# Kernel optimization log

Hardware: AMD Instinct MI355X
Metric: run time of the kernel (lower is better)

The kernel has to match this reference:

```python
import jax, jax.numpy as jnp
import numpy as np

N_NODES = 32768   # graph.num_nodes (coarse + fine levels)
N_ACTIVE = 28672  # rows of x (finest level)
N_EDGES = 229376  # avg degree ~7 (h3 k_ring + parent links)
C = 64            # node_channels
E_CH = 2          # edge_channels
HID = 128         # hidden_channels
L = 8             # num_layers


def _ln(x, g, b):
    # LayerNorm over last dim, eps=1e-5 (torch default)
    m = jnp.mean(x, axis=-1, keepdims=True)
    v = jnp.mean((x - m) ** 2, axis=-1, keepdims=True)
    return (x - m) * jax.lax.rsqrt(v + 1e-5) * g + b


def _ffn(x, w1, b1, w2, b2, g, bln, res_w=None, res_b=None):
    # FFN: norm(residual(x) + Linear-ReLU-Linear(x)); residual is Identity if in==out
    res = x @ res_w + res_b if res_w is not None else x
    h = jax.nn.relu(x @ w1 + b1) @ w2 + b2
    return _ln(res + h, g, bln)


def setup_inputs() -> dict:
    key = jax.random.key(0)
    ks = iter(jax.random.split(key, 64))

    def W(*s):
        return (0.02 * jax.random.normal(next(ks), s)).astype(jnp.float32)

    inp = {}
    inp['x'] = jax.random.normal(next(ks), (N_ACTIVE, C), jnp.float32)
    inp['edge_index'] = jax.random.randint(next(ks), (2, N_EDGES), 0, N_NODES)
    inp['edge_attr'] = jax.random.uniform(next(ks), (N_EDGES, E_CH), jnp.float32)
    # EdgeModel FFN: in = 2*C + E_CH -> out = E_CH (residual Linear since in != out)
    ein = 2 * C + E_CH
    inp['e_res_w'] = W(L, ein, E_CH); inp['e_res_b'] = jnp.zeros((L, E_CH), jnp.float32)
    inp['e_w1'] = W(L, ein, HID);     inp['e_b1'] = jnp.zeros((L, HID), jnp.float32)
    inp['e_w2'] = W(L, HID, E_CH);    inp['e_b2'] = jnp.zeros((L, E_CH), jnp.float32)
    inp['e_ln_g'] = jnp.ones((L, E_CH), jnp.float32); inp['e_ln_b'] = jnp.zeros((L, E_CH), jnp.float32)
    # NodeModel mlp_1: in = out = C + E_CH (residual Identity)
    m1 = C + E_CH
    inp['n1_w1'] = W(L, m1, HID);  inp['n1_b1'] = jnp.zeros((L, HID), jnp.float32)
    inp['n1_w2'] = W(L, HID, m1);  inp['n1_b2'] = jnp.zeros((L, m1), jnp.float32)
    inp['n1_ln_g'] = jnp.ones((L, m1), jnp.float32); inp['n1_ln_b'] = jnp.zeros((L, m1), jnp.float32)
    # NodeModel mlp_2: in = 2*C + E_CH -> out = C (residual Linear)
    inp['n2_res_w'] = W(L, ein, C); inp['n2_res_b'] = jnp.zeros((L, C), jnp.float32)
    inp['n2_w1'] = W(L, ein, HID);  inp['n2_b1'] = jnp.zeros((L, HID), jnp.float32)
    inp['n2_w2'] = W(L, HID, C);    inp['n2_b2'] = jnp.zeros((L, C), jnp.float32)
    inp['n2_ln_g'] = jnp.ones((L, C), jnp.float32); inp['n2_ln_b'] = jnp.zeros((L, C), jnp.float32)
    return inp


def reference(x, edge_index, edge_attr,
              e_res_w, e_res_b, e_w1, e_b1, e_w2, e_b2, e_ln_g, e_ln_b,
              n1_w1, n1_b1, n1_w2, n1_b2, n1_ln_g, n1_ln_b,
              n2_res_w, n2_res_b, n2_w1, n2_b1, n2_w2, n2_b2, n2_ln_g, n2_ln_b):
    pad = N_NODES - x.shape[0]
    nodes = jnp.concatenate([jnp.zeros((pad, x.shape[1]), x.dtype), x], axis=0)
    edges = edge_attr
    row, col = edge_index[0], edge_index[1]
    # per-node in-degree for scatter-mean (clamped to 1 so isolated nodes get 0)
    cnt = jnp.maximum(
        jax.ops.segment_sum(jnp.ones((N_EDGES,), x.dtype), col, num_segments=N_NODES), 1.0
    )[:, None]
    for l in range(L):
        src = nodes[row]   # [E, C]
        dst = nodes[col]   # [E, C]
        # EdgeModel: edge_mlp(cat(src, dest, edge_attr)) + edge_attr
        edges = _ffn(jnp.concatenate([src, dst, edges], axis=1),
                     e_w1[l], e_b1[l], e_w2[l], e_b2[l], e_ln_g[l], e_ln_b[l],
                     e_res_w[l], e_res_b[l]) + edges
        # NodeModel: mlp1 on cat(x[row], edge_attr), scatter-mean onto col
        m = _ffn(jnp.concatenate([src, edges], axis=1),
                 n1_w1[l], n1_b1[l], n1_w2[l], n1_b2[l], n1_ln_g[l], n1_ln_b[l])
        agg = jax.ops.segment_sum(m, col, num_segments=N_NODES) / cnt
        nodes = _ffn(jnp.concatenate([nodes, agg], axis=1),
                     n2_w1[l], n2_b1[l], n2_w2[l], n2_b2[l], n2_ln_g[l], n2_ln_b[l],
                     n2_res_w[l], n2_res_b[l]) + nodes
    return nodes[pad:]
```

## Files before the change

### kernel.cpp

```cpp
#include <hip/hip_runtime.h>

#define NN    32768
#define NACT  28672
#define NPAD  4096
#define NEDGE 229376
#define NLAY  8

#define WOFF_T0 0
#define WOFF_T1 18432
#define WOFF_T2 26624
#define WOFF_T3 36864
#define WOFF_T4 61440
#define WLO     69632
#define WLAYER  139264

typedef __attribute__((ext_vector_type(8))) short s16x8;
typedef __attribute__((ext_vector_type(8))) _Float16 f16x8;
typedef __attribute__((ext_vector_type(4))) float f32x4;
typedef unsigned short ushort_t;

#define MFMAH(a,b,c) __builtin_amdgcn_mfma_f32_16x16x32_f16((a),(b),(c),0,0,0)
#define INV2048 4.8828125e-4f

__device__ __forceinline__ unsigned short f2h(float f){
  union { _Float16 h; unsigned short u; } v; v.h = (_Float16)f; return v.u;
}
__device__ __forceinline__ float h2f(unsigned short u){
  union { unsigned short u; _Float16 h; } v; v.u = u; return (float)v.h;
}
__device__ __forceinline__ void split16(float a, unsigned short& h, unsigned short& r){
  float hf = 0.f; unsigned short hu = 0;
  if (__builtin_fabsf(a) >= 6.1035156e-5f){ hu = f2h(a); hf = h2f(hu); }
  h = hu;
  r = f2h((a - hf) * 2048.0f);
}
__device__ __forceinline__ void split8v(const float* v, s16x8& h, s16x8& r){
  #pragma unroll
  for (int i=0;i<8;++i){
    unsigned short hh, rr; split16(v[i], hh, rr);
    h[i] = (short)hh; r[i] = (short)rr;
  }
}

__global__ void k_pack(const float* __restrict__ ew1, const float* __restrict__ eresw,
                       const float* __restrict__ n1w1, const float* __restrict__ n1w2,
                       const float* __restrict__ n2w1, const float* __restrict__ n2resw,
                       const float* __restrict__ n2w2,
                       unsigned short* __restrict__ wfrag){
  const int l = blockIdx.y, T = blockIdx.z;
  int KT, NT, off;
  if (T==0){ KT=4; NT=9;  off=WOFF_T0; }
  else if (T==1){ KT=2; NT=8;  off=WOFF_T1; }
  else if (T==2){ KT=4; NT=5;  off=WOFF_T2; }
  else if (T==3){ KT=4; NT=12; off=WOFF_T3; }
  else          { KT=4; NT=4;  off=WOFF_T4; }
  const int f = blockIdx.x*256 + threadIdx.x;
  if (f >= KT*NT*64) return;
  const int lane = f & 63;
  const int fn = f >> 6;
  const int nt = fn % NT, ks = fn / NT;
  const int n  = nt*16 + (lane & 15);
  const int kb = ks*32 + (lane >> 4)*8;
  s16x8 vh, vl;
  #pragma unroll
  for (int i=0;i<8;++i){
    const int k = kb + i;
    float w = 0.f;
    if (T==0){
      if (n < 128)      w = ew1[((size_t)l*130 + k)*128 + n];
      else if (n < 130) w = eresw[((size_t)l*130 + k)*2 + (n-128)];
    } else if (T==1){
      w = n1w1[((size_t)l*66 + k)*128 + n];
    } else if (T==2){
      if (n < 66) w = n1w2[((size_t)l*128 + k)*66 + n];
    } else if (T==3){
      if (n < 128) w = n2w1[((size_t)l*130 + k)*128 + n];
      else         w = n2resw[((size_t)l*130 + k)*64 + (n-128)];
    } else {
      w = n2w2[((size_t)l*128 + k)*64 + n];
    }
    unsigned short hh, rr; split16(w, hh, rr);
    vh[i] = (short)hh; vl[i] = (short)rr;
  }
  *(s16x8*)(wfrag + (size_t)l*WLAYER + off + (size_t)f*8) = vh;
  *(s16x8*)(wfrag + (size_t)l*WLAYER + off + WLO + (size_t)f*8) = vl;
}

__global__ void k_init(const float* __restrict__ x, const float* __restrict__ ea,
                       float* __restrict__ nodes, float* __restrict__ edges,
                       int* __restrict__ cnt,
                       ushort_t* __restrict__ nh, ushort_t* __restrict__ nr){
  const int i = blockIdx.x*256 + threadIdx.x;
  const float v = (i >= NPAD*64) ? x[i - NPAD*64] : 0.f;
  nodes[i] = v;
  if (nh){
    unsigned short us, ur; split16(v, us, ur);
    nh[i] = us; nr[i] = ur;
  }
  if (i < NEDGE*2) edges[i] = ea[i];
  if (i < NN) cnt[i] = 0;
}

__global__ void k_count(const int* __restrict__ ei, int* __restrict__ cnt){
  const int e = blockIdx.x*256 + threadIdx.x;
  if (e < NEDGE) atomicAdd(&cnt[ei[NEDGE + e]], 1);
}

__global__ void k_inv(const int* __restrict__ cnt, float* __restrict__ invc,
                      int* __restrict__ fill){
  const int n = blockIdx.x*256 + threadIdx.x;
  if (n < NN){ invc[n] = 1.0f / (float)max(cnt[n], 1); fill[n] = 0; }
}

__global__ void k_scan(const int* __restrict__ cnt, int* __restrict__ row_start){
  __shared__ int part[256];
  const int t = threadIdx.x;
  int s = 0;
  for (int i=0;i<128;++i) s += cnt[t*128+i];
  part[t] = s;
  __syncthreads();
  if (t == 0){
    int run = 0;
    for (int i=0;i<256;++i){ const int v = part[i]; part[i] = run; run += v; }
  }
  __syncthreads();
  int base = part[t];
  for (int i=0;i<128;++i){ row_start[t*128+i] = base; base += cnt[t*128+i]; }
  if (t == 255) row_start[NN] = base;
}

__global__ void k_place(const int* __restrict__ ei, const int* __restrict__ row_start,
                        int* __restrict__ fill, int* __restrict__ ssrc,
                        int* __restrict__ sdst, int* __restrict__ seid){
  const int e = blockIdx.x*256 + threadIdx.x;
  if (e >= NEDGE) return;
  const int d = ei[NEDGE + e];
  const int pos = row_start[d] + atomicAdd(&fill[d], 1);
  ssrc[pos] = ei[e];
  sdst[pos] = d;
  seid[pos] = e;
}

__global__ void k_sortb(const int* __restrict__ row_start,
                        int* __restrict__ seid, int* __restrict__ ssrc){
  const int n = blockIdx.x*256 + threadIdx.x;
  if (n >= NN) return;
  const int rs = row_start[n], re = row_start[n+1];
  for (int i = rs+1; i < re; ++i){
    const int e = seid[i], s = ssrc[i];
    int j = i-1;
    while (j >= rs && seid[j] > e){ seid[j+1]=seid[j]; ssrc[j+1]=ssrc[j]; --j; }
    seid[j+1] = e; ssrc[j+1] = s;
  }
}

__global__ void k_perm(const float* __restrict__ ea, const int* __restrict__ seid,
                       float* __restrict__ edges){
  const int e = blockIdx.x*256 + threadIdx.x;
  if (e < NEDGE){
    const int o = seid[e];
    ((float2*)edges)[e] = ((const float2*)ea)[o];
  }
}

__global__ void k_zero_agg(float* __restrict__ agg64, float* __restrict__ agg2){
  const int i = blockIdx.x*256 + threadIdx.x;
  agg64[i] = 0.f;
  if (i < NN*2) agg2[i] = 0.f;
}

__global__ __launch_bounds__(256)
void k_agg(const float* __restrict__ medge64, const float* __restrict__ medge2,
           const int* __restrict__ row_start, const int* __restrict__ cnt,
           ushort_t* __restrict__ agg_h, ushort_t* __restrict__ agg_r,
           float* __restrict__ agg2){
  const int n = blockIdx.x*4 + (threadIdx.x >> 6);
  const int lane = threadIdx.x & 63;
  const int rs = row_start[n], re = row_start[n+1];
  const float cf = (float)max(cnt[n], 1);
  float a = 0.f, b = 0.f;
  for (int r = rs; r < re; ++r){
    a = __fadd_rn(a, medge64[(size_t)r*64 + lane]);
    if (lane < 2) b = __fadd_rn(b, medge2[(size_t)r*2 + lane]);
  }
  const float t = a / cf;
  unsigned short th, tr; split16(t, th, tr);
  agg_h[(size_t)n*64 + lane] = th;
  agg_r[(size_t)n*64 + lane] = tr;
  if (lane < 2) agg2[(size_t)n*2 + lane] = b / cf;
}

__global__ __launch_bounds__(256,3)
void k_edge(const int* __restrict__ sidx, const int* __restrict__ didx,
            float* __restrict__ edges,
            const float* __restrict__ nodes,
            const ushort_t* __restrict__ nh, const ushort_t* __restrict__ nr,
            const unsigned short* __restrict__ wf,
            float* __restrict__ agg64, float* __restrict__ agg2,
            float* __restrict__ medge64, float* __restrict__ medge2,
            const float* __restrict__ eb1, const float* __restrict__ ew2,
            const float* __restrict__ eb2, const float* __restrict__ eresb,
            const float* __restrict__ elng, const float* __restrict__ elnb,
            const float* __restrict__ ew1_tail,
            const float* __restrict__ eresw_tail,
            const float* __restrict__ n1w1_tail,
            const float* __restrict__ n1b1, const float* __restrict__ n1b2,
            const float* __restrict__ n1lng, const float* __restrict__ n1lnb)
{
  __shared__ __align__(16) unsigned char sAh[64*128];
  __shared__ __align__(16) unsigned char sAl[64*128];
  __shared__ __align__(16) unsigned char sBH[64*256];
  __shared__ __align__(16) unsigned char sH2l[64*256];
  __shared__ float sEold[64][2];
  __shared__ int   sCol[64];

  const int tid = threadIdx.x;
  const int ebase = blockIdx.x * 64;

  {
    const int r = (tid & 127) >> 1;
    const int half = tid & 1;
    const int es = ebase + r;
    const int swz = (r & 7) << 4;
    if (tid < 128){
      const int sn = sidx[es];
      if (nh){
        const ushort_t* hp = nh + (size_t)sn*64;
        const ushort_t* rp = nr + (size_t)sn*64;
        #pragma unroll
        for (int cc = 0; cc < 4; ++cc){
          const int c = half*4 + cc;
          const int o = r*128 + ((c*16) ^ swz);
          *(s16x8*)&sAh[o] = *(const s16x8*)(hp + c*8);
          *(s16x8*)&sAl[o] = *(const s16x8*)(rp + c*8);
        }
      } else {
        const float4* sp = (const float4*)(nodes + (size_t)sn*64);
        #pragma unroll
        for (int cc = 0; cc < 4; ++cc){
          const int c = half*4 + cc;
          const float4 f0 = sp[2*c], f1 = sp[2*c+1];
          float v[8] = {f0.x,f0.y,f0.z,f0.w,f1.x,f1.y,f1.z,f1.w};
          s16x8 hh, rr; split8v(v, hh, rr);
          const int o = r*128 + ((c*16) ^ swz);
          *(s16x8*)&sAh[o] = hh;
          *(s16x8*)&sAl[o] = rr;
        }
      }
    } else {
      const int dn = didx[es];
      if (nh){
        const ushort_t* hp = nh + (size_t)dn*64;
        const ushort_t* rp = nr + (size_t)dn*64;
        #pragma unroll
        for (int cc = 0; cc < 4; ++cc){
          const int c = half*4 + cc;
          const int o = r*128 + ((c*16) ^ swz);
          *(s16x8*)&sBH[o] = *(const s16x8*)(hp + c*8);
          *(s16x8*)&sBH[8192 + o] = *(const s16x8*)(rp + c*8);
        }
      } else {
        const float4* dp = (const float4*)(nodes + (size_t)dn*64);
        #pragma unroll
        for (int cc = 0; cc < 4; ++cc){
          const int c = half*4 + cc;
          const float4 f0 = dp[2*c], f1 = dp[2*c+1];
          float v[8] = {f0.x,f0.y,f0.z,f0.w,f1.x,f1.y,f1.z,f1.w};
          s16x8 hh, rr; split8v(v, hh, rr);
          const int o = r*128 + ((c*16) ^ swz);
          *(s16x8*)&sBH[o] = hh;
          *(s16x8*)&sBH[8192 + o] = rr;
        }
      }
      if (half == 0){
        const float2 ev = *(const float2*)(edges + (size_t)es*2);
        sEold[r][0] = ev.x; sEold[r][1] = ev.y;
        sCol[r] = dn;
      }
    }
  }
  __syncthreads();

  const int lane  = tid & 63;
  const int wv    = tid >> 6;
  const int colj  = lane & 15;
  const int g     = lane >> 4;
  const int rowA0 = wv*16 + colj;
  const int mrow0 = wv*16 + g*4;

  float e0r[4], e1r[4];
  #pragma unroll
  for (int r=0; r<4; ++r){
    const int m = mrow0 + r;
    e0r[r] = sEold[m][0]; e1r[r] = sEold[m][1];
  }

  f32x4 acc1[9];
  #pragma unroll
  for (int i=0;i<9;++i) acc1[i] = f32x4{0,0,0,0};
  {
    #pragma unroll
    for (int half = 0; half < 2; ++half){
      const int nt0 = half*5;
      const int NTH = half ? 4 : 5;
      f32x4 accR[5];
      #pragma unroll
      for (int i=0;i<5;++i) accR[i] = f32x4{0,0,0,0};
      #pragma unroll
      for (int ks = 0; ks < 4; ++ks){
        const int ch = (ks&1)*4 + g;
        const unsigned char* pH = (ks<2) ? sAh : sBH;
        const unsigned char* pL = (ks<2) ? sAl : (sBH + 8192);
        const int o0 = rowA0*128 + ((ch*16) ^ ((rowA0&7)<<4));
        const f16x8 ah = *(const f16x8*)&pH[o0];
        const f16x8 ar = *(const f16x8*)&pL[o0];
        const f16x8* bh = (const f16x8*)(wf + WOFF_T0) + (ks*9 + nt0)*64 + lane;
        const f16x8* bl = (const f16x8*)(wf + WOFF_T0 + WLO) + (ks*9 + nt0)*64 + lane;
        #pragma unroll
        for (int t = 0; t < 5; ++t){
          if (t >= NTH) break;
          const f16x8 b1 = bh[t*64];
          const f16x8 b2 = bl[t*64];
          acc1[nt0+t] = MFMAH(ah, b1, acc1[nt0+t]);
          accR[t]     = MFMAH(ar, b1, accR[t]);
          accR[t]     = MFMAH(ah, b2, accR[t]);
        }
      }
      #pragma unroll
      for (int t=0; t<5; ++t){
        if (t >= NTH) break;
        #pragma unroll
        for (int r=0; r<4; ++r)
          acc1[nt0+t][r] += accR[t][r] * INV2048;
      }
    }
    #pragma unroll
    for (int nt=0; nt<9; ++nt){
      const int j = nt*16 + colj;
      float w0, w1;
      if (nt < 8){ w0 = ew1_tail[j]; w1 = ew1_tail[128 + j]; }
      else { w0 = (colj<2) ? eresw_tail[colj] : 0.f; w1 = (colj<2) ? eresw_tail[2+colj] : 0.f; }
      #pragma unroll
      for (int r=0; r<4; ++r)
        acc1[nt][r] += e0r[r]*w0 + e1r[r]*w1;
    }
  }

  float enew[4][2];
  {
    float2 w2v[8]; float b1v[8];
    #pragma unroll
    for (int nt=0; nt<8; ++nt){
      const int j = nt*16 + colj;
      w2v[nt] = *(const float2*)(ew2 + (size_t)j*2);
      b1v[nt] = eb1[j];
    }
    const float rb0 = eresb[0], rb1 = eresb[1];
    const float g0 = elng[0], g1 = elng[1], lb0 = elnb[0], lb1 = elnb[1];
    const float bb0 = eb2[0], bb1 = eb2[1];
    #pragma unroll
    for (int r=0; r<4; ++r){
      float v0 = 0.f, v1 = 0.f;
      #pragma unroll
      for (int nt=0; nt<8; ++nt){
        const float h = fmaxf(acc1[nt][r] + b1v[nt], 0.f);
        v0 = fmaf(h, w2v[nt].x, v0);
        v1 = fmaf(h, w2v[nt].y, v1);
      }
      const float resv = acc1[8][r];
      if (colj == 0) v0 += resv + rb0;
      if (colj == 1) v1 += resv + rb1;
      #pragma unroll
      for (int mm=1; mm<16; mm<<=1){
        v0 += __shfl_xor(v0, mm, 64);
        v1 += __shfl_xor(v1, mm, 64);
      }
      v0 += bb0; v1 += bb1;
      const float m2 = __fmul_rn(__fadd_rn(v0, v1), 0.5f);
      const float d0 = __fsub_rn(v0, m2);
      const float d1 = __fsub_rn(v1, m2);
      const float var = __fmul_rn(__fadd_rn(__fmul_rn(d0,d0), __fmul_rn(d1,d1)), 0.5f);
      const float rstd = 1.0f / sqrtf(var + 1e-5f);
      const int m = mrow0 + r;
      const float e0 = __fadd_rn(__fadd_rn(__fmul_rn(__fmul_rn(d0, rstd), g0), lb0), e0r[r]);
      const float e1 = __fadd_rn(__fadd_rn(__fmul_rn(__fmul_rn(d1, rstd), g1), lb1), e1r[r]);
      enew[r][0] = e0; enew[r][1] = e1;
      if (colj == 0)
        *(float2*)(edges + (size_t)(ebase + m)*2) = make_float2(e0, e1);
    }
  }

  f32x4 acc2[8];
  #pragma unroll
  for (int i=0;i<8;++i) acc2[i] = f32x4{0,0,0,0};
  {
    #pragma unroll
    for (int half = 0; half < 2; ++half){
      const int nt0 = half*4;
      f32x4 accR[4];
      #pragma unroll
      for (int i=0;i<4;++i) accR[i] = f32x4{0,0,0,0};
      #pragma unroll
      for (int ks=0; ks<2; ++ks){
        const int ch = ks*4 + g;
        const int o0 = rowA0*128 + ((ch*16) ^ ((rowA0&7)<<4));
        const f16x8 ah = *(const f16x8*)&sAh[o0];
        const f16x8 ar = *(const f16x8*)&sAl[o0];
        const f16x8* bh = (const f16x8*)(wf + WOFF_T1) + (ks*8 + nt0)*64 + lane;
        const f16x8* bl = (const f16x8*)(wf + WOFF_T1 + WLO) + (ks*8 + nt0)*64 + lane;
        #pragma unroll
        for (int t = 0; t < 4; ++t){
          const f16x8 b1 = bh[t*64];
          const f16x8 b2 = bl[t*64];
          acc2[nt0+t] = MFMAH(ah, b1, acc2[nt0+t]);
          accR[t]     = MFMAH(ar, b1, accR[t]);
          accR[t]     = MFMAH(ah, b2, accR[t]);
        }
      }
      #pragma unroll
      for (int t=0; t<4; ++t)
        #pragma unroll
        for (int r=0; r<4; ++r)
          acc2[nt0+t][r] += accR[t][r] * INV2048;
    }
  }
  {
    #pragma unroll
    for (int nt=0; nt<8; ++nt){
      const int j = nt*16 + colj;
      const float w64 = n1w1_tail[j];
      const float w65 = n1w1_tail[128 + j];
      const float bb = n1b1[j];
      #pragma unroll
      for (int r=0; r<4; ++r){
        float h = acc2[nt][r] + enew[r][0]*w64 + enew[r][1]*w65 + bb;
        acc2[nt][r] = fmaxf(h, 0.f);
      }
    }
  }

  __syncthreads();

  {
    #pragma unroll
    for (int nt=0; nt<8; ++nt){
      const int j = nt*16 + colj;
      const int co = (j>>3)<<4, wi = (j&7)*2;
      #pragma unroll
      for (int r=0; r<4; ++r){
        const int m = mrow0 + r;
        unsigned short us, ur; split16(acc2[nt][r], us, ur);
        const int o = m*256 + ((co ^ ((m&7)<<4)) + wi);
        *(unsigned short*)&sBH[o]  = us;
        *(unsigned short*)&sH2l[o] = ur;
      }
    }
  }
  __syncthreads();

  f32x4 acc3[5], acc3R[5];
  #pragma unroll
  for (int i=0;i<5;++i){ acc3[i] = f32x4{0,0,0,0}; acc3R[i] = f32x4{0,0,0,0}; }
  #pragma unroll
  for (int ks=0; ks<4; ++ks){
    const int ch = ks*4 + g;
    const f16x8 a0 = *(const f16x8*)&sBH[rowA0*256 + ((ch*16) ^ ((rowA0&7)<<4))];
    const f16x8* bh = (const f16x8*)(wf + WOFF_T2) + (ks*5)*64 + lane;
    const f16x8* bl = (const f16x8*)(wf + WOFF_T2 + WLO) + (ks*5)*64 + lane;
    #pragma unroll
    for (int nt = 0; nt < 5; ++nt){
      const f16x8 b1 = bh[nt*64];
      const f16x8 b2 = bl[nt*64];
      acc3[nt]  = MFMAH(a0, b1, acc3[nt]);
      acc3R[nt] = MFMAH(a0, b2, acc3R[nt]);
    }
  }
  #pragma unroll
  for (int ks=0; ks<4; ++ks){
    const int ch = ks*4 + g;
    const f16x8 a0 = *(const f16x8*)&sH2l[rowA0*256 + ((ch*16) ^ ((rowA0&7)<<4))];
    const f16x8* bh = (const f16x8*)(wf + WOFF_T2) + (ks*5)*64 + lane;
    #pragma unroll
    for (int nt = 0; nt < 5; ++nt){
      const f16x8 b1 = bh[nt*64];
      acc3R[nt] = MFMAH(a0, b1, acc3R[nt]);
    }
  }
  #pragma unroll
  for (int nt=0; nt<5; ++nt)
    #pragma unroll
    for (int r=0; r<4; ++r)
      acc3[nt][r] += acc3R[nt][r] * INV2048;

  {
    float b2v[5], lgv[5], lbv[5];
    #pragma unroll
    for (int nt=0; nt<5; ++nt){
      const int j = nt*16 + colj;
      const bool ok = j < 66;
      b2v[nt] = ok ? n1b2[j]  : 0.f;
      lgv[nt] = ok ? n1lng[j] : 0.f;
      lbv[nt] = ok ? n1lnb[j] : 0.f;
    }
    #pragma unroll
    for (int r=0; r<4; ++r){
      const int m = mrow0 + r;
      float v[5]; float sum = 0.f;
      #pragma unroll
      for (int nt=0; nt<5; ++nt){
        const int j = nt*16 + colj;
        float xv = 0.f;
        if (j < 64){
          const int o = m*128 + (((((j>>3)<<4)) ^ ((m&7)<<4)) + (j&7)*2);
          const float resd = h2f(*(const unsigned short*)&sAh[o])
                           + h2f(*(const unsigned short*)&sAl[o]) * INV2048;
          xv = __fadd_rn(resd, __fadd_rn(acc3[nt][r], b2v[nt]));
        } else if (j < 66){
          xv = __fadd_rn(enew[r][j-64], __fadd_rn(acc3[nt][r], b2v[nt]));
        }
        v[nt] = xv;
        sum += xv;
      }
      #pragma unroll
      for (int mm=1; mm<16; mm<<=1) sum += __shfl_xor(sum, mm, 64);
      const float mean = sum / 66.0f;
      float d[5]; float sq = 0.f;
      #pragma unroll
      for (int nt=0; nt<5; ++nt){
        const int j = nt*16 + colj;
        d[nt] = (j < 66) ? __fsub_rn(v[nt], mean) : 0.f;
        sq = __fadd_rn(sq, __fmul_rn(d[nt], d[nt]));
      }
      #pragma unroll
      for (int mm=1; mm<16; mm<<=1) sq += __shfl_xor(sq, mm, 64);
      const float var  = sq / 66.0f;
      const float rstd = 1.0f / sqrtf(var + 1e-5f);
      if (medge64){
        float* m64 = medge64 + (size_t)(ebase + m)*64;
        #pragma unroll
        for (int nt=0; nt<4; ++nt)
          m64[nt*16 + colj] = __fadd_rn(__fmul_rn(__fmul_rn(d[nt], rstd), lgv[nt]), lbv[nt]);
        if (colj < 2)
          medge2[(size_t)(ebase + m)*2 + colj] =
            __fadd_rn(__fmul_rn(__fmul_rn(d[4], rstd), lgv[4]), lbv[4]);
      } else {
        float* a64 = agg64 + (size_t)sCol[m]*64;
        #pragma unroll
        for (int nt=0; nt<4; ++nt)
          atomicAdd(a64 + nt*16 + colj, __fadd_rn(__fmul_rn(__fmul_rn(d[nt], rstd), lgv[nt]), lbv[nt]));
        if (colj < 2)
          atomicAdd(agg2 + (size_t)sCol[m]*2 + colj,
                    __fadd_rn(__fmul_rn(__fmul_rn(d[4], rstd), lgv[4]), lbv[4]));
      }
    }
  }
}

__global__ __launch_bounds__(256,3)
void k_node(float* __restrict__ nodes,
            ushort_t* __restrict__ nh, ushort_t* __restrict__ nr,
            const float* __restrict__ agg64,
            const ushort_t* __restrict__ agg_h, const ushort_t* __restrict__ agg_r,
            const float* __restrict__ agg2,
            const float* __restrict__ invc,
            const unsigned short* __restrict__ wf,
            const float* __restrict__ b1, const float* __restrict__ resb,
            const float* __restrict__ b2, const float* __restrict__ lng,
            const float* __restrict__ lnb,
            const float* __restrict__ n2w1_tail,
            const float* __restrict__ n2resw_tail)
{
  __shared__ __align__(16) unsigned char sAh[64*128];
  __shared__ __align__(16) unsigned char sAl[64*128];
  __shared__ __align__(16) unsigned char sBH[64*256];
  __shared__ __align__(16) unsigned char sH3l[64*256];
  __shared__ float sAgg2[64][2];

  const int tid = threadIdx.x;
  const int nbase = blockIdx.x * 64;

  {
    const int r = (tid & 127) >> 1;
    const int half = tid & 1;
    const int node = nbase + r;
    const int swz = (r & 7) << 4;
    if (tid < 128){
      if (nh){
        const ushort_t* hp = nh + (size_t)node*64;
        const ushort_t* rp = nr + (size_t)node*64;
        #pragma unroll
        for (int cc = 0; cc < 4; ++cc){
          const int c = half*4 + cc;
          const int o = r*128 + ((c*16) ^ swz);
          *(s16x8*)&sAh[o] = *(const s16x8*)(hp + c*8);
          *(s16x8*)&sAl[o] = *(const s16x8*)(rp + c*8);
        }
      } else {
        const float4* sp = (const float4*)(nodes + (size_t)node*64);
        #pragma unroll
        for (int cc = 0; cc < 4; ++cc){
          const int c = half*4 + cc;
          const float4 f0 = sp[2*c], f1 = sp[2*c+1];
          float v[8] = {f0.x,f0.y,f0.z,f0.w,f1.x,f1.y,f1.z,f1.w};
          s16x8 hh, rr; split8v(v, hh, rr);
          const int o = r*128 + ((c*16) ^ swz);
          *(s16x8*)&sAh[o] = hh;
          *(s16x8*)&sAl[o] = rr;
        }
      }
    } else {
      if (agg_h){
        const ushort_t* hp = agg_h + (size_t)node*64;
        const ushort_t* rp = agg_r + (size_t)node*64;
        #pragma unroll
        for (int cc = 0; cc < 4; ++cc){
          const int c = half*4 + cc;
          const int o = r*128 + ((c*16) ^ swz);
          *(s16x8*)&sBH[o] = *(const s16x8*)(hp + c*8);
          *(s16x8*)&sBH[8192 + o] = *(const s16x8*)(rp + c*8);
        }
        if (half == 0){
          sAgg2[r][0] = agg2[(size_t)node*2];
          sAgg2[r][1] = agg2[(size_t)node*2+1];
        }
      } else {
        const float iv = invc[node];
        const float* a64 = agg64 + (size_t)node*64;
        #pragma unroll
        for (int cc = 0; cc < 4; ++cc){
          const int c = half*4 + cc;
          float v[8];
          #pragma unroll
          for (int i=0;i<8;++i) v[i] = a64[c*8+i]*iv;
          s16x8 hh, rr; split8v(v, hh, rr);
          const int o = r*128 + ((c*16) ^ swz);
          *(s16x8*)&sBH[o] = hh;
          *(s16x8*)&sBH[8192 + o] = rr;
        }
        if (half == 0){
          sAgg2[r][0] = agg2[(size_t)node*2]*iv;
          sAgg2[r][1] = agg2[(size_t)node*2+1]*iv;
        }
      }
    }
  }
  __syncthreads();

  const int lane  = tid & 63;
  const int wv    = tid >> 6;
  const int colj  = lane & 15;
  const int g     = lane >> 4;
  const int rowA0 = wv*16 + colj;
  const int mrow0 = wv*16 + g*4;

  float a0r[4], a1r[4];
  #pragma unroll
  for (int r=0; r<4; ++r){
    const int m = mrow0 + r;
    a0r[r] = sAgg2[m][0]; a1r[r] = sAgg2[m][1];
  }

  f32x4 acc1[12];
  #pragma unroll
  for (int i=0;i<12;++i) acc1[i] = f32x4{0,0,0,0};
  #pragma unroll
  for (int half = 0; half < 2; ++half){
    f32x4 aR[6];
    #pragma unroll
    for (int i=0;i<6;++i) aR[i] = f32x4{0,0,0,0};
    #pragma unroll
    for (int ks = 0; ks < 4; ++ks){
      const int ch = (ks&1)*4 + g;
      const unsigned char* pH = (ks<2) ? sAh : sBH;
      const unsigned char* pL = (ks<2) ? sAl : (sBH + 8192);
      const int o0 = rowA0*128 + ((ch*16) ^ ((rowA0&7)<<4));
      const f16x8 ah = *(const f16x8*)&pH[o0];
      const f16x8 ar = *(const f16x8*)&pL[o0];
      const f16x8* bh = (const f16x8*)(wf + WOFF_T3) + (ks*12 + half*6)*64 + lane;
      const f16x8* bl = (const f16x8*)(wf + WOFF_T3 + WLO) + (ks*12 + half*6)*64 + lane;
      #pragma unroll
      for (int t = 0; t < 6; ++t){
        const int nt = half*6 + t;
        const f16x8 b1 = bh[t*64];
        const f16x8 b2 = bl[t*64];
        acc1[nt] = MFMAH(ah, b1, acc1[nt]);
        aR[t]    = MFMAH(ar, b1, aR[t]);
        aR[t]    = MFMAH(ah, b2, aR[t]);
      }
    }
    #pragma unroll
    for (int t=0;t<6;++t)
      #pragma unroll
      for (int r=0; r<4; ++r)
        acc1[half*6+t][r] += aR[t][r] * INV2048;
  }
  {
    #pragma unroll
    for (int nt=0; nt<12; ++nt){
      const int j = nt*16 + colj;
      float w0, w1;
      if (j < 128){ w0 = n2w1_tail[j]; w1 = n2w1_tail[128 + j]; }
      else { w0 = n2resw_tail[j-128]; w1 = n2resw_tail[64 + (j-128)]; }
      #pragma unroll
      for (int r=0; r<4; ++r)
        acc1[nt][r] += a0r[r]*w0 + a1r[r]*w1;
    }
  }
  {
    #pragma unroll
    for (int nt=0; nt<8; ++nt){
      const float bb = b1[nt*16 + colj];
      #pragma unroll
      for (int r=0; r<4; ++r)
        acc1[nt][r] = fmaxf(acc1[nt][r] + bb, 0.f);
    }
  }

  __syncthreads();

  {
    #pragma unroll
    for (int nt=0; nt<8; ++nt){
      const int j = nt*16 + colj;
      const int co = (j>>3)<<4, wi = (j&7)*2;
      #pragma unroll
      for (int r=0; r<4; ++r){
        const int m = mrow0 + r;
        unsigned short us, ur; split16(acc1[nt][r], us, ur);
        const int o = m*256 + ((co ^ ((m&7)<<4)) + wi);
        *(unsigned short*)&sBH[o]  = us;
        *(unsigned short*)&sH3l[o] = ur;
      }
    }
  }
  __syncthreads();

  f32x4 acc2[4], acc2R[4];
  #pragma unroll
  for (int i=0;i<4;++i){ acc2[i] = f32x4{0,0,0,0}; acc2R[i] = f32x4{0,0,0,0}; }
  #pragma unroll
  for (int ks=0; ks<4; ++ks){
    const int ch = ks*4 + g;
    const f16x8 a0 = *(const f16x8*)&sBH[rowA0*256 + ((ch*16) ^ ((rowA0&7)<<4))];
    const f16x8* bh = (const f16x8*)(wf + WOFF_T4) + (ks*4)*64 + lane;
    const f16x8* bl = (const f16x8*)(wf + WOFF_T4 + WLO) + (ks*4)*64 + lane;
    #pragma unroll
    for (int nt = 0; nt < 4; ++nt){
      const f16x8 b1 = bh[nt*64];
      const f16x8 b2 = bl[nt*64];
      acc2[nt]  = MFMAH(a0, b1, acc2[nt]);
      acc2R[nt] = MFMAH(a0, b2, acc2R[nt]);
    }
  }
  #pragma unroll
  for (int ks=0; ks<4; ++ks){
    const int ch = ks*4 + g;
    const f16x8 a0 = *(const f16x8*)&sH3l[rowA0*256 + ((ch*16) ^ ((rowA0&7)<<4))];
    const f16x8* bh = (const f16x8*)(wf + WOFF_T4) + (ks*4)*64 + lane;
    #pragma unroll
    for (int nt = 0; nt < 4; ++nt){
      const f16x8 b1 = bh[nt*64];
      acc2R[nt] = MFMAH(a0, b1, acc2R[nt]);
    }
  }
  #pragma unroll
  for (int nt=0; nt<4; ++nt)
    #pragma unroll
    for (int r=0; r<4; ++r)
      acc2[nt][r] += acc2R[nt][r] * INV2048;

  {
    float b2v[4], rbv[4], lgv[4], lbv[4];
    #pragma unroll
    for (int nt=0; nt<4; ++nt){
      const int j = nt*16 + colj;
      b2v[nt] = b2[j]; rbv[nt] = resb[j]; lgv[nt] = lng[j]; lbv[nt] = lnb[j];
    }
    #pragma unroll
    for (int r=0; r<4; ++r){
      const int m = mrow0 + r;
      const int node = nbase + m;
      float v[4]; float sum = 0.f;
      #pragma unroll
      for (int nt=0; nt<4; ++nt){
        const float resi = __fadd_rn(acc1[8+nt][r], rbv[nt]);
        const float hh   = __fadd_rn(acc2[nt][r], b2v[nt]);
        const float xv = __fadd_rn(resi, hh);
        v[nt] = xv; sum += xv;
      }
      #pragma unroll
      for (int mm=1; mm<16; mm<<=1) sum += __shfl_xor(sum, mm, 64);
      const float mean = sum / 64.0f;
      float d[4]; float sq = 0.f;
      #pragma unroll
      for (int nt=0; nt<4; ++nt){
        d[nt] = __fsub_rn(v[nt], mean);
        sq = __fadd_rn(sq, __fmul_rn(d[nt], d[nt]));
      }
      #pragma unroll
      for (int mm=1; mm<16; mm<<=1) sq += __shfl_xor(sq, mm, 64);
      const float var  = sq / 64.0f;
      const float rstd = 1.0f / sqrtf(var + 1e-5f);
      #pragma unroll
      for (int nt=0; nt<4; ++nt){
        const int j = nt*16 + colj;
        const size_t idx = (size_t)node*64 + j;
        const float lnout = __fadd_rn(__fmul_rn(__fmul_rn(d[nt], rstd), lgv[nt]), lbv[nt]);
        const float out = __fadd_rn(lnout, nodes[idx]);
        nodes[idx] = out;
        if (nh){
          unsigned short us, ur; split16(out, us, ur);
          nh[idx] = us; nr[idx] = ur;
        }
      }
    }
  }
}

__global__ void k_copy(const float* __restrict__ nodes, float* __restrict__ out){
  const int i = blockIdx.x*256 + threadIdx.x;
  if (i < NACT*16)
    ((float4*)out)[i] = ((const float4*)nodes)[NPAD*16 + i];
}

extern "C" void kernel_launch(void* const* d_in, const int* in_sizes, int n_in,
                              void* d_out, int out_size, void* d_ws, size_t ws_size,
                              hipStream_t stream){
  const float* x       = (const float*)d_in[0];
  const int*   ei      = (const int*)  d_in[1];
  const float* eattr   = (const float*)d_in[2];
  const float* e_res_w = (const float*)d_in[3];
  const float* e_res_b = (const float*)d_in[4];
  const float* e_w1    = (const float*)d_in[5];
  const float* e_b1    = (const float*)d_in[6];
  const float* e_w2    = (const float*)d_in[7];
  const float* e_b2    = (const float*)d_in[8];
  const float* e_ln_g  = (const float*)d_in[9];
  const float* e_ln_b  = (const float*)d_in[10];
  const float* n1_w1   = (const float*)d_in[11];
  const float* n1_b1   = (const float*)d_in[12];
  const float* n1_w2   = (const float*)d_in[13];
  const float* n1_b2   = (const float*)d_in[14];
  const float* n1_ln_g = (const float*)d_in[15];
  const float* n1_ln_b = (const float*)d_in[16];
  const float* n2_res_w= (const float*)d_in[17];
  const float* n2_res_b= (const float*)d_in[18];
  const float* n2_w1   = (const float*)d_in[19];
  const float* n2_b1   = (const float*)d_in[20];
  const float* n2_w2   = (const float*)d_in[21];
  const float* n2_b2   = (const float*)d_in[22];
  const float* n2_ln_g = (const float*)d_in[23];
  const float* n2_ln_b = (const float*)d_in[24];

  if (ws_size < 21364736u) return;

  char* ws = (char*)d_ws;
  float*          nodes = (float*)(ws + 0);
  float*          edges = (float*)(ws + 8388608);
  float*          agg64 = (float*)(ws + 10223616);
  ushort_t*       agg_h = (ushort_t*)(ws + 10223616);
  ushort_t*       agg_r = (ushort_t*)(ws + 14417920);
  float*          agg2  = (float*)(ws + 18612224);
  int*            cnt   = (int*)(ws + 18874368);
  float*          invc  = (float*)(ws + 19005440);
  unsigned short* wfrag = (unsigned short*)(ws + 19136512);
  int*   row_start = (int*)(ws + 21364736);
  int*   fill      = (int*)(ws + 21496064);
  int*   ssrc      = (int*)(ws + 21627136);
  int*   sdst      = (int*)(ws + 22544640);
  int*   seid      = (int*)(ws + 23462144);
  float* medge64   = (float*)(ws + 24379648);
  float* medge2    = (float*)(ws + 83099904);
  ushort_t* nodes_h = (ushort_t*)(ws + 84934912);
  ushort_t* nodes_r = (ushort_t*)(ws + 89129216);

  const bool fast  = ws_size >= 84934912u;
  const bool fast2 = ws_size >= 93323520u;

  ushort_t* nh = fast2 ? nodes_h : nullptr;
  ushort_t* nr = fast2 ? nodes_r : nullptr;

  k_pack<<<dim3(12,8,5),256,0,stream>>>(e_w1, e_res_w, n1_w1, n1_w2, n2_w1, n2_res_w, n2_w2, wfrag);
  k_init<<<8192,256,0,stream>>>(x, eattr, nodes, edges, cnt, nh, nr);
  k_count<<<896,256,0,stream>>>(ei, cnt);
  k_inv<<<128,256,0,stream>>>(cnt, invc, fast ? fill : cnt );

  const int* sidx = ei;
  const int* didx = ei + NEDGE;
  if (fast){
    k_scan<<<1,256,0,stream>>>(cnt, row_start);
    k_place<<<896,256,0,stream>>>(ei, row_start, fill, ssrc, sdst, seid);
    k_sortb<<<128,256,0,stream>>>(row_start, seid, ssrc);
    k_perm<<<896,256,0,stream>>>(eattr, seid, edges);
    sidx = ssrc; didx = sdst;
  }

  for (int l = 0; l < NLAY; ++l){
    if (!fast) k_zero_agg<<<8192,256,0,stream>>>(agg64, agg2);
    k_edge<<<3584,256,0,stream>>>(sidx, didx, edges, nodes, nh, nr,
        wfrag + (size_t)l*WLAYER, agg64, agg2,
        fast ? medge64 : nullptr, fast ? medge2 : nullptr,
        e_b1 + l*128, e_w2 + l*256, e_b2 + l*2, e_res_b + l*2, e_ln_g + l*2, e_ln_b + l*2,
        e_w1 + ((size_t)l*130 + 128)*128,
        e_res_w + ((size_t)l*130 + 128)*2,
        n1_w1 + ((size_t)l*66 + 64)*128,
        n1_b1 + l*128, n1_b2 + l*66, n1_ln_g + l*66, n1_ln_b + l*66);
    if (fast) k_agg<<<8192,256,0,stream>>>(medge64, medge2, row_start, cnt, agg_h, agg_r, agg2);
    k_node<<<512,256,0,stream>>>(nodes, nh, nr,
        fast ? nullptr : agg64,
        fast ? agg_h : nullptr, fast ? agg_r : nullptr, agg2,
        fast ? nullptr : invc,
        wfrag + (size_t)l*WLAYER,
        n2_b1 + l*128, n2_res_b + l*64, n2_b2 + l*64, n2_ln_g + l*64, n2_ln_b + l*64,
        n2_w1 + ((size_t)l*130 + 128)*128,
        n2_res_w + ((size_t)l*130 + 128)*64);
  }
  k_copy<<<1792,256,0,stream>>>(nodes, (float*)d_out);
}
```

Baseline: 1.367 ms.

## Fuse CSR aggregation into node kernel and halve LDS to raise occupancy

Measured after the change: 1.843 ms. 1.35x slower.

```diff
diff --git a/kernel.cpp b/kernel.cpp
--- a/kernel.cpp
+++ b/kernel.cpp
@@ -169,28 +169,7 @@
   if (i < NN*2) agg2[i] = 0.f;
 }
 
-__global__ __launch_bounds__(256)
-void k_agg(const float* __restrict__ medge64, const float* __restrict__ medge2,
-           const int* __restrict__ row_start, const int* __restrict__ cnt,
-           ushort_t* __restrict__ agg_h, ushort_t* __restrict__ agg_r,
-           float* __restrict__ agg2){
-  const int n = blockIdx.x*4 + (threadIdx.x >> 6);
-  const int lane = threadIdx.x & 63;
-  const int rs = row_start[n], re = row_start[n+1];
-  const float cf = (float)max(cnt[n], 1);
-  float a = 0.f, b = 0.f;
-  for (int r = rs; r < re; ++r){
-    a = __fadd_rn(a, medge64[(size_t)r*64 + lane]);
-    if (lane < 2) b = __fadd_rn(b, medge2[(size_t)r*2 + lane]);
-  }
-  const float t = a / cf;
-  unsigned short th, tr; split16(t, th, tr);
-  agg_h[(size_t)n*64 + lane] = th;
-  agg_r[(size_t)n*64 + lane] = tr;
-  if (lane < 2) agg2[(size_t)n*2 + lane] = b / cf;
-}
-
-__global__ __launch_bounds__(256,3)
+__global__ __launch_bounds__(256,4)
 void k_edge(const int* __restrict__ sidx, const int* __restrict__ didx,
             float* __restrict__ edges,
             const float* __restrict__ nodes,
@@ -209,8 +188,8 @@
 {
   __shared__ __align__(16) unsigned char sAh[64*128];
   __shared__ __align__(16) unsigned char sAl[64*128];
-  __shared__ __align__(16) unsigned char sBH[64*256];
-  __shared__ __align__(16) unsigned char sH2l[64*256];
+  __shared__ __align__(16) unsigned char sBh[64*128];
+  __shared__ __align__(16) unsigned char sBl[64*128];
   __shared__ float sEold[64][2];
   __shared__ int   sCol[64];
 
@@ -256,8 +235,8 @@
         for (int cc = 0; cc < 4; ++cc){
           const int c = half*4 + cc;
           const int o = r*128 + ((c*16) ^ swz);
-          *(s16x8*)&sBH[o] = *(const s16x8*)(hp + c*8);
-          *(s16x8*)&sBH[8192 + o] = *(const s16x8*)(rp + c*8);
+          *(s16x8*)&sBh[o] = *(const s16x8*)(hp + c*8);
+          *(s16x8*)&sBl[o] = *(const s16x8*)(rp + c*8);
         }
       } else {
         const float4* dp = (const float4*)(nodes + (size_t)dn*64);
@@ -268,8 +247,8 @@
           float v[8] = {f0.x,f0.y,f0.z,f0.w,f1.x,f1.y,f1.z,f1.w};
           s16x8 hh, rr; split8v(v, hh, rr);
           const int o = r*128 + ((c*16) ^ swz);
-          *(s16x8*)&sBH[o] = hh;
-          *(s16x8*)&sBH[8192 + o] = rr;
+          *(s16x8*)&sBh[o] = hh;
+          *(s16x8*)&sBl[o] = rr;
         }
       }
       if (half == 0){
@@ -309,8 +288,8 @@
       #pragma unroll
       for (int ks = 0; ks < 4; ++ks){
         const int ch = (ks&1)*4 + g;
-        const unsigned char* pH = (ks<2) ? sAh : sBH;
-        const unsigned char* pL = (ks<2) ? sAl : (sBH + 8192);
+        const unsigned char* pH = (ks<2) ? sAh : sBh;
+        const unsigned char* pL = (ks<2) ? sAl : sBl;
         const int o0 = rowA0*128 + ((ch*16) ^ ((rowA0&7)<<4));
         const f16x8 ah = *(const f16x8*)&pH[o0];
         const f16x8 ar = *(const f16x8*)&pL[o0];
@@ -439,51 +418,44 @@
     }
   }
 
-  __syncthreads();
-
-  {
-    #pragma unroll
-    for (int nt=0; nt<8; ++nt){
-      const int j = nt*16 + colj;
-      const int co = (j>>3)<<4, wi = (j&7)*2;
+  f32x4 acc3[5], acc3R[5];
+  #pragma unroll
+  for (int i=0;i<5;++i){ acc3[i] = f32x4{0,0,0,0}; acc3R[i] = f32x4{0,0,0,0}; }
+  #pragma unroll
+  for (int c = 0; c < 2; ++c){
+    __syncthreads();
+    #pragma unroll
+    for (int ntl=0; ntl<4; ++ntl){
+      const int nt = c*4 + ntl;
+      const int jc = ntl*16 + colj;
+      const int co = (jc>>3)<<4, wi = (jc&7)*2;
       #pragma unroll
       for (int r=0; r<4; ++r){
         const int m = mrow0 + r;
         unsigned short us, ur; split16(acc2[nt][r], us, ur);
-        const int o = m*256 + ((co ^ ((m&7)<<4)) + wi);
-        *(unsigned short*)&sBH[o]  = us;
-        *(unsigned short*)&sH2l[o] = ur;
-      }
-    }
-  }
-  __syncthreads();
-
-  f32x4 acc3[5], acc3R[5];
-  #pragma unroll
-  for (int i=0;i<5;++i){ acc3[i] = f32x4{0,0,0,0}; acc3R[i] = f32x4{0,0,0,0}; }
-  #pragma unroll
-  for (int ks=0; ks<4; ++ks){
-    const int ch = ks*4 + g;
-    const f16x8 a0 = *(const f16x8*)&sBH[rowA0*256 + ((ch*16) ^ ((rowA0&7)<<4))];
-    const f16x8* bh = (const f16x8*)(wf + WOFF_T2) + (ks*5)*64 + lane;
-    const f16x8* bl = (const f16x8*)(wf + WOFF_T2 + WLO) + (ks*5)*64 + lane;
-    #pragma unroll
-    for (int nt = 0; nt < 5; ++nt){
-      const f16x8 b1 = bh[nt*64];
-      const f16x8 b2 = bl[nt*64];
-      acc3[nt]  = MFMAH(a0, b1, acc3[nt]);
-      acc3R[nt] = MFMAH(a0, b2, acc3R[nt]);
-    }
-  }
-  #pragma unroll
-  for (int ks=0; ks<4; ++ks){
-    const int ch = ks*4 + g;
-    const f16x8 a0 = *(const f16x8*)&sH2l[rowA0*256 + ((ch*16) ^ ((rowA0&7)<<4))];
-    const f16x8* bh = (const f16x8*)(wf + WOFF_T2) + (ks*5)*64 + lane;
-    #pragma unroll
-    for (int nt = 0; nt < 5; ++nt){
-      const f16x8 b1 = bh[nt*64];
-      acc3R[nt] = MFMAH(a0, b1, acc3R[nt]);
+        const int o = m*128 + ((co ^ ((m&7)<<4)) + wi);
+        *(unsigned short*)&sBh[o] = us;
+        *(unsigned short*)&sBl[o] = ur;
+      }
+    }
+    __syncthreads();
+    #pragma unroll
+    for (int ksl=0; ksl<2; ++ksl){
+      const int ks = c*2 + ksl;
+      const int ch = ksl*4 + g;
+      const int o0 = rowA0*128 + ((ch*16) ^ ((rowA0&7)<<4));
+      const f16x8 ah = *(const f16x8*)&sBh[o0];
+      const f16x8 al = *(const f16x8*)&sBl[o0];
+      const f16x8* bh = (const f16x8*)(wf + WOFF_T2) + (ks*5)*64 + lane;
+      const f16x8* bl = (const f16x8*)(wf + WOFF_T2 + WLO) + (ks*5)*64 + lane;
+      #pragma unroll
+      for (int nt = 0; nt < 5; ++nt){
+        const f16x8 b1 = bh[nt*64];
+        const f16x8 b2 = bl[nt*64];
+        acc3[nt]  = MFMAH(ah, b1, acc3[nt]);
+        acc3R[nt] = MFMAH(ah, b2, acc3R[nt]);
+        acc3R[nt] = MFMAH(al, b1, acc3R[nt]);
+      }
     }
   }
   #pragma unroll
@@ -556,12 +528,12 @@
   }
 }
 
-__global__ __launch_bounds__(256,3)
+__global__ __launch_bounds__(256,4)
 void k_node(float* __restrict__ nodes,
             ushort_t* __restrict__ nh, ushort_t* __restrict__ nr,
-            const float* __restrict__ agg64,
-            const ushort_t* __restrict__ agg_h, const ushort_t* __restrict__ agg_r,
-            const float* __restrict__ agg2,
+            const float* __restrict__ medge64, const float* __restrict__ medge2,
+            const int* __restrict__ row_start, const int* __restrict__ cntp,
+            const float* __restrict__ agg64, const float* __restrict__ agg2,
             const float* __restrict__ invc,
             const unsigned short* __restrict__ wf,
             const float* __restrict__ b1, const float* __restrict__ resb,
@@ -572,8 +544,8 @@
 {
   __shared__ __align__(16) unsigned char sAh[64*128];
   __shared__ __align__(16) unsigned char sAl[64*128];
-  __shared__ __align__(16) unsigned char sBH[64*256];
-  __shared__ __align__(16) unsigned char sH3l[64*256];
+  __shared__ __align__(16) unsigned char sBh[64*128];
+  __shared__ __align__(16) unsigned char sBl[64*128];
   __shared__ float sAgg2[64][2];
 
   const int tid = threadIdx.x;
@@ -609,19 +581,36 @@
         }
       }
     } else {
-      if (agg_h){
-        const ushort_t* hp = agg_h + (size_t)node*64;
-        const ushort_t* rp = agg_r + (size_t)node*64;
+      if (medge64){
+        const int rs = row_start[node], re = row_start[node+1];
+        const float cf = (float)max(cntp[node], 1);
         #pragma unroll
         for (int cc = 0; cc < 4; ++cc){
           const int c = half*4 + cc;
+          float a[8];
+          #pragma unroll
+          for (int i=0;i<8;++i) a[i] = 0.f;
+          for (int rr = rs; rr < re; ++rr){
+            const float* mr = medge64 + (size_t)rr*64 + c*8;
+            #pragma unroll
+            for (int i=0;i<8;++i) a[i] = __fadd_rn(a[i], mr[i]);
+          }
+          float v[8];
+          #pragma unroll
+          for (int i=0;i<8;++i) v[i] = a[i] / cf;
+          s16x8 hh, rr2; split8v(v, hh, rr2);
           const int o = r*128 + ((c*16) ^ swz);
-          *(s16x8*)&sBH[o] = *(const s16x8*)(hp + c*8);
-          *(s16x8*)&sBH[8192 + o] = *(const s16x8*)(rp + c*8);
+          *(s16x8*)&sBh[o] = hh;
+          *(s16x8*)&sBl[o] = rr2;
         }
         if (half == 0){
-          sAgg2[r][0] = agg2[(size_t)node*2];
-          sAgg2[r][1] = agg2[(size_t)node*2+1];
+          float b0 = 0.f, b1s = 0.f;
+          for (int rr = rs; rr < re; ++rr){
+            b0  = __fadd_rn(b0,  medge2[(size_t)rr*2]);
+            b1s = __fadd_rn(b1s, medge2[(size_t)rr*2+1]);
+          }
+          sAgg2[r][0] = b0 / cf;
+          sAgg2[r][1] = b1s / cf;
         }
       } else {
         const float iv = invc[node];
@@ -634,8 +623,8 @@
           for (int i=0;i<8;++i) v[i] = a64[c*8+i]*iv;
           s16x8 hh, rr; split8v(v, hh, rr);
           const int o = r*128 + ((c*16) ^ swz);
-          *(s16x8*)&sBH[o] = hh;
-          *(s16x8*)&sBH[8192 + o] = rr;
+          *(s16x8*)&sBh[o] = hh;
+          *(s16x8*)&sBl[o] = rr;
         }
         if (half == 0){
           sAgg2[r][0] = agg2[(size_t)node*2]*iv;
@@ -671,8 +660,8 @@
     #pragma unroll
     for (int ks = 0; ks < 4; ++ks){
       const int ch = (ks&1)*4 + g;
-      const unsigned char* pH = (ks<2) ? sAh : sBH;
-      const unsigned char* pL = (ks<2) ? sAl : (sBH + 8192);
+      const unsigned char* pH = (ks<2) ? sAh : sBh;
+      const unsigned char* pL = (ks<2) ? sAl : sBl;
       const int o0 = rowA0*128 + ((ch*16) ^ ((rowA0&7)<<4));
       const f16x8 ah = *(const f16x8*)&pH[o0];
       const f16x8 ar = *(const f16x8*)&pL[o0];
@@ -716,51 +705,44 @@
     }
   }
 
-  __syncthreads();
-
-  {
-    #pragma unroll
-    for (int nt=0; nt<8; ++nt){
-      const int j = nt*16 + colj;
-      const int co = (j>>3)<<4, wi = (j&7)*2;
+  f32x4 acc2[4], acc2R[4];
+  #pragma unroll
+  for (int i=0;i<4;++i){ acc2[i] = f32x4{0,0,0,0}; acc2R[i] = f32x4{0,0,0,0}; }
+  #pragma unroll
+  for (int c = 0; c < 2; ++c){
+    __syncthreads();
+    #pragma unroll
+    for (int ntl=0; ntl<4; ++ntl){
+      const int nt = c*4 + ntl;
+      const int jc = ntl*16 + colj;
+      const int co = (jc>>3)<<4, wi = (jc&7)*2;
       #pragma unroll
       for (int r=0; r<4; ++r){
         const int m = mrow0 + r;
         unsigned short us, ur; split16(acc1[nt][r], us, ur);
-        const int o = m*256 + ((co ^ ((m&7)<<4)) + wi);
-        *(unsigned short*)&sBH[o]  = us;
-        *(unsigned short*)&sH3l[o] = ur;
-      }
-    }
-  }
-  __syncthreads();
-
-  f32x4 acc2[4], acc2R[4];
-  #pragma unroll
-  for (int i=0;i<4;++i){ acc2[i] = f32x4{0,0,0,0}; acc2R[i] = f32x4{0,0,0,0}; }
-  #pragma unroll
-  for (int ks=0; ks<4; ++ks){
-    const int ch = ks*4 + g;
-    const f16x8 a0 = *(const f16x8*)&sBH[rowA0*256 + ((ch*16) ^ ((rowA0&7)<<4))];
-    const f16x8* bh = (const f16x8*)(wf + WOFF_T4) + (ks*4)*64 + lane;
-    const f16x8* bl = (const f16x8*)(wf + WOFF_T4 + WLO) + (ks*4)*64 + lane;
-    #pragma unroll
-    for (int nt = 0; nt < 4; ++nt){
-      const f16x8 b1 = bh[nt*64];
-      const f16x8 b2 = bl[nt*64];
-      acc2[nt]  = MFMAH(a0, b1, acc2[nt]);
-      acc2R[nt] = MFMAH(a0, b2, acc2R[nt]);
-    }
-  }
-  #pragma unroll
-  for (int ks=0; ks<4; ++ks){
-    const int ch = ks*4 + g;
-    const f16x8 a0 = *(const f16x8*)&sH3l[rowA0*256 + ((ch*16) ^ ((rowA0&7)<<4))];
-    const f16x8* bh = (const f16x8*)(wf + WOFF_T4) + (ks*4)*64 + lane;
-    #pragma unroll
-    for (int nt = 0; nt < 4; ++nt){
-      const f16x8 b1 = bh[nt*64];
-      acc2R[nt] = MFMAH(a0, b1, acc2R[nt]);
+        const int o = m*128 + ((co ^ ((m&7)<<4)) + wi);
+        *(unsigned short*)&sBh[o] = us;
+        *(unsigned short*)&sBl[o] = ur;
+      }
+    }
+    __syncthreads();
+    #pragma unroll
+    for (int ksl=0; ksl<2; ++ksl){
+      const int ks = c*2 + ksl;
+      const int ch = ksl*4 + g;
+      const int o0 = rowA0*128 + ((ch*16) ^ ((rowA0&7)<<4));
+      const f16x8 ah = *(const f16x8*)&sBh[o0];
+      const f16x8 al = *(const f16x8*)&sBl[o0];
+      const f16x8* bh = (const f16x8*)(wf + WOFF_T4) + (ks*4)*64 + lane;
+      const f16x8* bl = (const f16x8*)(wf + WOFF_T4 + WLO) + (ks*4)*64 + lane;
+      #pragma unroll
+      for (int nt = 0; nt < 4; ++nt){
+        const f16x8 b1 = bh[nt*64];
+        const f16x8 b2 = bl[nt*64];
+        acc2[nt]  = MFMAH(ah, b1, acc2[nt]);
+        acc2R[nt] = MFMAH(ah, b2, acc2R[nt]);
+        acc2R[nt] = MFMAH(al, b1, acc2R[nt]);
+      }
     }
   }
   #pragma unroll
@@ -858,8 +840,6 @@
   float*          nodes = (float*)(ws + 0);
   float*          edges = (float*)(ws + 8388608);
   float*          agg64 = (float*)(ws + 10223616);
-  ushort_t*       agg_h = (ushort_t*)(ws + 10223616);
-  ushort_t*       agg_r = (ushort_t*)(ws + 14417920);
   float*          agg2  = (float*)(ws + 18612224);
   int*            cnt   = (int*)(ws + 18874368);
   float*          invc  = (float*)(ws + 19005440);
@@ -905,10 +885,10 @@
         e_res_w + ((size_t)l*130 + 128)*2,
         n1_w1 + ((size_t)l*66 + 64)*128,
         n1_b1 + l*128, n1_b2 + l*66, n1_ln_g + l*66, n1_ln_b + l*66);
-    if (fast) k_agg<<<8192,256,0,stream>>>(medge64, medge2, row_start, cnt, agg_h, agg_r, agg2);
     k_node<<<512,256,0,stream>>>(nodes, nh, nr,
-        fast ? nullptr : agg64,
-        fast ? agg_h : nullptr, fast ? agg_r : nullptr, agg2,
+        fast ? medge64 : nullptr, fast ? medge2 : nullptr,
+        fast ? row_start : nullptr, cnt,
+        agg64, agg2,
         fast ? nullptr : invc,
         wfrag + (size_t)l*WLAYER,
         n2_b1 + l*128, n2_res_b + l*64, n2_b2 + l*64, n2_ln_g + l*64, n2_ln_b + l*64,
```
